# Kernel tuning notes

Measured on AMD Instinct MI355X. Metric: run time of the kernel, lower is better.

The kernel has to match this reference:

```python
import jax, jax.numpy as jnp
import numpy as np

D_MODEL = 1024
N_HEADS = 16
D_HEAD = D_MODEL // N_HEADS
D_FF = 4096
B, S = 4, 1024
EPS = 1e-12


def layer_norm(x, gamma, beta):
    # Faithful to the torch module: unbiased std (ddof=1) and division by (std + eps).
    mean = jnp.mean(x, axis=-1, keepdims=True)
    var = jnp.sum((x - mean) ** 2, axis=-1, keepdims=True) / (x.shape[-1] - 1)
    std = jnp.sqrt(var)
    return gamma * (x - mean) / (std + EPS) + beta


def setup_inputs() -> dict:
    key = jax.random.key(0)
    ks = jax.random.split(key, 10)
    sc = lambda fan_in: 1.0 / np.sqrt(fan_in)
    inp = {
        "x": jax.random.normal(ks[0], (B, S, D_MODEL), dtype=jnp.float32),
        "ln1_g": jnp.ones((D_MODEL,), jnp.float32),
        "ln1_b": jnp.zeros((D_MODEL,), jnp.float32),
        "wq": jax.random.normal(ks[1], (D_MODEL, D_MODEL), jnp.float32) * sc(D_MODEL),
        "bq": jnp.zeros((D_MODEL,), jnp.float32),
        "wk": jax.random.normal(ks[2], (D_MODEL, D_MODEL), jnp.float32) * sc(D_MODEL),
        "bk": jnp.zeros((D_MODEL,), jnp.float32),
        "wv": jax.random.normal(ks[3], (D_MODEL, D_MODEL), jnp.float32) * sc(D_MODEL),
        "bv": jnp.zeros((D_MODEL,), jnp.float32),
        "ln2_g": jnp.ones((D_MODEL,), jnp.float32),
        "ln2_b": jnp.zeros((D_MODEL,), jnp.float32),
        "w1": jax.random.normal(ks[4], (D_FF, D_MODEL), jnp.float32) * sc(D_MODEL),
        "b1": jnp.zeros((D_FF,), jnp.float32),
        "w2": jax.random.normal(ks[5], (D_MODEL, D_FF), jnp.float32) * sc(D_FF),
        "b2": jnp.zeros((D_MODEL,), jnp.float32),
    }
    return inp


def reference(x, ln1_g, ln1_b, wq, bq, wk, bk, wv, bv, ln2_g, ln2_b, w1, b1, w2, b2):
    Bsz, Sq, D = x.shape
    residual = x
    h = layer_norm(x, ln1_g, ln1_b)
    # QKV projections (no output projection in the original module)
    q = (h @ wq.T + bq).reshape(Bsz, Sq, N_HEADS, D_HEAD)
    k = (h @ wk.T + bk).reshape(Bsz, Sq, N_HEADS, D_HEAD)
    v = (h @ wv.T + bv).reshape(Bsz, Sq, N_HEADS, D_HEAD)
    scores = jnp.einsum("bqhd,bkhd->bhqk", q, k) / np.sqrt(D_HEAD)
    attn = jax.nn.softmax(scores, axis=-1)  # [B, H, S, S]
    ctx = jnp.einsum("bhqk,bkhd->bqhd", attn, v).reshape(Bsz, Sq, D)
    out = ctx + residual
    residual = out
    h2 = layer_norm(out, ln2_g, ln2_b)
    # 1x1 conv FFN == per-token MLP with ReLU (dropout inactive at eval)
    ff = jax.nn.relu(h2 @ w1.T + b1) @ w2.T + b2
    out = ff + residual
    # torch returns attn flattened head-major: [H*B, S, S]
    attn_ret = jnp.transpose(attn, (1, 0, 2, 3)).reshape(N_HEADS * Bsz, Sq, Sq)
    return out, attn_ret
```

## Files before the change

### kernel.cpp

```cpp
#include <hip/hip_runtime.h>
#include <cstdint>
#include <cstddef>

#define SEQ 1024
#define DM 1024
#define DF 4096
#define NH 16
#define DH 64
#define BSZ 4
#define NTOK (BSZ*SEQ)

typedef short s16x8 __attribute__((ext_vector_type(8)));
typedef float f32x4 __attribute__((ext_vector_type(4)));

__device__ __forceinline__ unsigned short f2bf(float f) {
  union { float f; unsigned u; } c; c.f = f;
  unsigned u = c.u;
  return (unsigned short)((u + 0x7fffu + ((u >> 16) & 1u)) >> 16);
}

__device__ __forceinline__ void gll16(const void* g, void* l) {
  __builtin_amdgcn_global_load_lds(
      (__attribute__((address_space(1))) void*)(g),
      (__attribute__((address_space(3))) void*)(l), 16, 0, 0);
}

template<int BM, int BN, int WM, int WN, int EPI>
__launch_bounds__(256)
__global__ void gemm_k(const unsigned short* __restrict__ A,
                       const unsigned short* __restrict__ W,
                       const float* __restrict__ bias,
                       void* __restrict__ outp,
                       const float* __restrict__ resid,
                       int nB, int K, int aRow, int wRow, int oRow,
                       long aY, long aZ, long wY, long wZ,
                       long oY, long oZ, long rY, long rZ, float scale) {
  constexpr int BK = 32;
  __shared__ unsigned short At[BM*BK];
  __shared__ unsigned short Wt[BN*BK];
  const int tid = threadIdx.x;
  const int mb = (int)blockIdx.x / nB, nb = (int)blockIdx.x % nB;
  const long aBase = (long)blockIdx.y*aY + (long)blockIdx.z*aZ + (long)mb*BM*aRow;
  const long wBase = (long)blockIdx.y*wY + (long)blockIdx.z*wZ + (long)nb*BN*wRow;
  const int wave = tid >> 6, lane = tid & 63;
  const int quad = lane >> 4, l16 = lane & 15;
  constexpr int WGN = BN / WN;
  const int wm = (wave / WGN) * WM, wn = (wave % WGN) * WN;
  constexpr int MT = WM/16, NT = WN/16;
  f32x4 acc[MT][NT] = {};
  const int srow = tid >> 2, skof = (tid & 3) * 8;

  for (int k0 = 0; k0 < K; k0 += BK) {
#pragma unroll
    for (int r = 0; r < BM; r += 64)
      gll16(A + aBase + (long)(r + srow)*aRow + k0 + skof, &At[(r + srow)*BK + skof]);
#pragma unroll
    for (int r = 0; r < BN; r += 64)
      gll16(W + wBase + (long)(r + srow)*wRow + k0 + skof, &Wt[(r + srow)*BK + skof]);
    __syncthreads();
    s16x8 af[MT];
#pragma unroll
    for (int mt = 0; mt < MT; ++mt)
      af[mt] = *(const s16x8*)&At[(wm + mt*16 + l16)*BK + quad*8];
#pragma unroll
    for (int nt = 0; nt < NT; ++nt) {
      s16x8 bfr = *(const s16x8*)&Wt[(wn + nt*16 + l16)*BK + quad*8];
#pragma unroll
      for (int mt = 0; mt < MT; ++mt)
        acc[mt][nt] = __builtin_amdgcn_mfma_f32_16x16x32_bf16(af[mt], bfr, acc[mt][nt], 0, 0, 0);
    }
    __syncthreads();
  }

  const long oBase = (long)blockIdx.y*oY + (long)blockIdx.z*oZ;
  const long rBase = (long)blockIdx.y*rY + (long)blockIdx.z*rZ;
#pragma unroll
  for (int mt = 0; mt < MT; ++mt) {
#pragma unroll
    for (int nt = 0; nt < NT; ++nt) {
      const int gn = nb*BN + wn + nt*16 + l16;
      const float bv = bias ? bias[gn] : 0.f;
#pragma unroll
      for (int r = 0; r < 4; ++r) {
        const int gm = mb*BM + wm + mt*16 + quad*4 + r;
        float v = acc[mt][nt][r] + bv;
        if (EPI == 0) {
          ((unsigned short*)outp)[oBase + (long)gm*oRow + gn] = f2bf(v * scale);
        } else if (EPI == 1) {
          ((unsigned short*)outp)[oBase + (long)gm*oRow + gn] = f2bf(v > 0.f ? v : 0.f);
        } else if (EPI == 2) {
          const int bb = gm >> 10, s = gm & 1023;
          ((unsigned short*)outp)[(long)bb*DM*SEQ + (long)gn*SEQ + s] = f2bf(v);
        } else if (EPI == 3) {
          const long o = oBase + (long)gm*oRow + gn;
          ((float*)outp)[o] = v + resid[rBase + (long)gm*oRow + gn];
        } else {
          ((float*)outp)[oBase + (long)gm*oRow + gn] = v;
        }
      }
    }
  }
}

__launch_bounds__(256)
__global__ void ln_k(const float* __restrict__ x, const float* __restrict__ g,
                     const float* __restrict__ bta, unsigned short* __restrict__ out) {
  const int row = blockIdx.x, t = threadIdx.x;
  const float4 v = ((const float4*)(x + (long)row*DM))[t];
  __shared__ float red[4];
  float s = v.x + v.y + v.z + v.w;
#pragma unroll
  for (int o = 32; o; o >>= 1) s += __shfl_down(s, o);
  if ((t & 63) == 0) red[t >> 6] = s;
  __syncthreads();
  const float mean = (red[0] + red[1] + red[2] + red[3]) * (1.f/1024.f);
  __syncthreads();
  const float dx = v.x - mean, dy = v.y - mean, dz = v.z - mean, dw = v.w - mean;
  float sq = dx*dx + dy*dy + dz*dz + dw*dw;
#pragma unroll
  for (int o = 32; o; o >>= 1) sq += __shfl_down(sq, o);
  if ((t & 63) == 0) red[t >> 6] = sq;
  __syncthreads();
  const float var = (red[0] + red[1] + red[2] + red[3]) * (1.f/1023.f);
  const float inv = 1.f / (sqrtf(var) + 1e-12f);
  const float4 gv = ((const float4*)g)[t];
  const float4 bv = ((const float4*)bta)[t];
  ushort4 o4;
  o4.x = f2bf(gv.x * dx * inv + bv.x);
  o4.y = f2bf(gv.y * dy * inv + bv.y);
  o4.z = f2bf(gv.z * dz * inv + bv.z);
  o4.w = f2bf(gv.w * dw * inv + bv.w);
  ((ushort4*)(out + (long)row*DM))[t] = o4;
}

__launch_bounds__(256)
__global__ void cvt_k(const float* __restrict__ in, unsigned short* __restrict__ out, int n4) {
  const int i = blockIdx.x*256 + threadIdx.x;
  if (i < n4) {
    const float4 v = ((const float4*)in)[i];
    ushort4 o; o.x = f2bf(v.x); o.y = f2bf(v.y); o.z = f2bf(v.z); o.w = f2bf(v.w);
    ((ushort4*)out)[i] = o;
  }
}

__launch_bounds__(256)
__global__ void attn_k(const unsigned short* __restrict__ Q,
                       const unsigned short* __restrict__ Kb,
                       float* __restrict__ attn_f,
                       unsigned short* __restrict__ attn_b) {
  const int b = blockIdx.y, h = blockIdx.z;
  const int q0 = blockIdx.x * 16;
  const int wave = threadIdx.x >> 6, lane = threadIdx.x & 63;
  const int quad = lane >> 4, l16 = lane & 15;
  const unsigned short* Qb = Q + (long)b*SEQ*DM + h*DH;
  const unsigned short* Kh = Kb + (long)b*SEQ*DM + h*DH;
  s16x8 af[2];
#pragma unroll
  for (int ks = 0; ks < 2; ++ks)
    af[ks] = *(const s16x8*)&Qb[(long)(q0 + l16)*DM + ks*32 + quad*8];
  f32x4 acc[16];
#pragma unroll
  for (int nt = 0; nt < 16; ++nt) acc[nt] = (f32x4){0.f, 0.f, 0.f, 0.f};
  for (int nt = 0; nt < 16; ++nt) {
    const int kc = wave*256 + nt*16 + l16;
#pragma unroll
    for (int ks = 0; ks < 2; ++ks) {
      const s16x8 bfr = *(const s16x8*)&Kh[(long)kc*DM + ks*32 + quad*8];
      acc[nt] = __builtin_amdgcn_mfma_f32_16x16x32_bf16(af[ks], bfr, acc[nt], 0, 0, 0);
    }
  }
  __shared__ float red[4][16];
  float rmax[4];
#pragma unroll
  for (int r = 0; r < 4; ++r) {
    float m = -3e38f;
#pragma unroll
    for (int nt = 0; nt < 16; ++nt) m = fmaxf(m, acc[nt][r]);
#pragma unroll
    for (int o = 1; o < 16; o <<= 1) m = fmaxf(m, __shfl_xor(m, o));
    rmax[r] = m;
  }
  if (l16 == 0) {
#pragma unroll
    for (int r = 0; r < 4; ++r) red[wave][quad*4 + r] = rmax[r];
  }
  __syncthreads();
#pragma unroll
  for (int r = 0; r < 4; ++r)
    rmax[r] = fmaxf(fmaxf(red[0][quad*4+r], red[1][quad*4+r]),
                    fmaxf(red[2][quad*4+r], red[3][quad*4+r]));
  __syncthreads();
#pragma unroll
  for (int r = 0; r < 4; ++r) {
    float s = 0.f;
#pragma unroll
    for (int nt = 0; nt < 16; ++nt) {
      const float e = __expf(acc[nt][r] - rmax[r]);
      acc[nt][r] = e; s += e;
    }
#pragma unroll
    for (int o = 1; o < 16; o <<= 1) s += __shfl_xor(s, o);
    if (l16 == 0) red[wave][quad*4 + r] = s;
  }
  __syncthreads();
  const long obase = (long)(h*BSZ + b)*SEQ*SEQ;
#pragma unroll
  for (int r = 0; r < 4; ++r) {
    const float tot = red[0][quad*4+r] + red[1][quad*4+r] + red[2][quad*4+r] + red[3][quad*4+r];
    const float inv = 1.f / tot;
    const long rowoff = obase + (long)(q0 + quad*4 + r)*SEQ;
#pragma unroll
    for (int nt = 0; nt < 16; ++nt) {
      const int col = wave*256 + nt*16 + l16;
      const float v = acc[nt][r] * inv;
      attn_f[rowoff + col] = v;
      attn_b[rowoff + col] = f2bf(v);
    }
  }
}

extern "C" void kernel_launch(void* const* d_in, const int* in_sizes, int n_in,
                              void* d_out, int out_size, void* d_ws, size_t ws_size,
                              hipStream_t stream) {
  const float* x    = (const float*)d_in[0];
  const float* ln1g = (const float*)d_in[1];
  const float* ln1b = (const float*)d_in[2];
  const float* wq   = (const float*)d_in[3];
  const float* bq   = (const float*)d_in[4];
  const float* wk   = (const float*)d_in[5];
  const float* bk   = (const float*)d_in[6];
  const float* wv   = (const float*)d_in[7];
  const float* bv   = (const float*)d_in[8];
  const float* ln2g = (const float*)d_in[9];
  const float* ln2b = (const float*)d_in[10];
  const float* w1   = (const float*)d_in[11];
  const float* b1   = (const float*)d_in[12];
  const float* w2   = (const float*)d_in[13];
  const float* b2   = (const float*)d_in[14];
  float* out    = (float*)d_out;
  float* attn_f = out + (long)NTOK*DM;

  uint8_t* p = (uint8_t*)d_ws;
  auto alloc = [&](size_t bytes) {
    uint8_t* r = p; p += (bytes + 255) & ~(size_t)255; return r;
  };
  unsigned short* hbuf  = (unsigned short*)alloc((size_t)NTOK*DM*2);
  unsigned short* qbuf  = (unsigned short*)alloc((size_t)NTOK*DM*2);
  unsigned short* kbuf  = (unsigned short*)alloc((size_t)NTOK*DM*2);
  unsigned short* vt    = (unsigned short*)alloc((size_t)BSZ*DM*SEQ*2);
  unsigned short* h2    = (unsigned short*)alloc((size_t)NTOK*DM*2);
  unsigned short* f1    = (unsigned short*)alloc((size_t)NTOK*DF*2);
  float*          out1  = (float*)alloc((size_t)NTOK*DM*4);
  unsigned short* attnb = (unsigned short*)alloc((size_t)NH*BSZ*SEQ*SEQ*2);
  unsigned short* wqb   = (unsigned short*)alloc((size_t)DM*DM*2);
  unsigned short* wkb   = (unsigned short*)alloc((size_t)DM*DM*2);
  unsigned short* wvb   = (unsigned short*)alloc((size_t)DM*DM*2);
  unsigned short* w1b   = (unsigned short*)alloc((size_t)DF*DM*2);
  unsigned short* w2b   = (unsigned short*)alloc((size_t)DM*DF*2);

  cvt_k<<<DM*DM/4/256, 256, 0, stream>>>(wq, wqb, DM*DM/4);
  cvt_k<<<DM*DM/4/256, 256, 0, stream>>>(wk, wkb, DM*DM/4);
  cvt_k<<<DM*DM/4/256, 256, 0, stream>>>(wv, wvb, DM*DM/4);
  cvt_k<<<DF*DM/4/256, 256, 0, stream>>>(w1, w1b, DF*DM/4);
  cvt_k<<<DM*DF/4/256, 256, 0, stream>>>(w2, w2b, DM*DF/4);

  ln_k<<<NTOK, 256, 0, stream>>>(x, ln1g, ln1b, hbuf);

  gemm_k<128,128,64,64,0><<<dim3((NTOK/128)*(DM/128)), 256, 0, stream>>>(
      hbuf, wqb, bq, qbuf, nullptr, DM/128, DM, DM, DM, DM,
      0,0,0,0,0,0,0,0, 0.125f);
  gemm_k<128,128,64,64,0><<<dim3((NTOK/128)*(DM/128)), 256, 0, stream>>>(
      hbuf, wkb, bk, kbuf, nullptr, DM/128, DM, DM, DM, DM,
      0,0,0,0,0,0,0,0, 1.f);
  gemm_k<128,128,64,64,2><<<dim3((NTOK/128)*(DM/128)), 256, 0, stream>>>(
      hbuf, wvb, bv, vt, nullptr, DM/128, DM, DM, DM, DM,
      0,0,0,0,0,0,0,0, 1.f);

  attn_k<<<dim3(SEQ/16, BSZ, NH), 256, 0, stream>>>(qbuf, kbuf, attn_f, attnb);

  gemm_k<128,64,32,64,3><<<dim3(SEQ/128, BSZ, NH), 256, 0, stream>>>(
      attnb, vt, nullptr, out1, x, 1, SEQ, SEQ, SEQ, DM,
      (long)SEQ*SEQ, (long)BSZ*SEQ*SEQ,
      (long)DM*SEQ, (long)DH*SEQ,
      (long)SEQ*DM, (long)DH,
      (long)SEQ*DM, (long)DH, 1.f);

  ln_k<<<NTOK, 256, 0, stream>>>(out1, ln2g, ln2b, h2);

  gemm_k<128,128,64,64,1><<<dim3((NTOK/128)*(DF/128)), 256, 0, stream>>>(
      h2, w1b, b1, f1, nullptr, DF/128, DM, DM, DM, DF,
      0,0,0,0,0,0,0,0, 1.f);

  gemm_k<128,128,64,64,3><<<dim3((NTOK/128)*(DM/128)), 256, 0, stream>>>(
      f1, w2b, b2, out, out1, DM/128, DF, DF, DF, DM,
      0,0,0,0,0,0,0,0, 1.f);
}
```

Before: 747.8 us.

## Fuse QKV GEMMs, weight conversions, and attention-times-V into attention kernel

After: 687.2 us. -8.1%, faster.

```diff
diff --git a/kernel.cpp b/kernel.cpp
--- a/kernel.cpp
+++ b/kernel.cpp
@@ -9,6 +9,7 @@
 #define DH 64
 #define BSZ 4
 #define NTOK (BSZ*SEQ)
+#define QKVSZ ((long)NTOK*DM)
 
 typedef short s16x8 __attribute__((ext_vector_type(8)));
 typedef float f32x4 __attribute__((ext_vector_type(4)));
@@ -17,6 +18,9 @@
   union { float f; unsigned u; } c; c.f = f;
   unsigned u = c.u;
   return (unsigned short)((u + 0x7fffu + ((u >> 16) & 1u)) >> 16);
+}
+__device__ __forceinline__ float bf2f(unsigned short b) {
+  union { unsigned u; float f; } c; c.u = ((unsigned)b) << 16; return c.f;
 }
 
 __device__ __forceinline__ void gll16(const void* g, void* l) {
@@ -33,15 +37,14 @@
                        void* __restrict__ outp,
                        const float* __restrict__ resid,
                        int nB, int K, int aRow, int wRow, int oRow,
-                       long aY, long aZ, long wY, long wZ,
-                       long oY, long oZ, long rY, long rZ, float scale) {
+                       float scale) {
   constexpr int BK = 32;
   __shared__ unsigned short At[BM*BK];
   __shared__ unsigned short Wt[BN*BK];
   const int tid = threadIdx.x;
   const int mb = (int)blockIdx.x / nB, nb = (int)blockIdx.x % nB;
-  const long aBase = (long)blockIdx.y*aY + (long)blockIdx.z*aZ + (long)mb*BM*aRow;
-  const long wBase = (long)blockIdx.y*wY + (long)blockIdx.z*wZ + (long)nb*BN*wRow;
+  const long aBase = (long)mb*BM*aRow;
+  const long wBase = (long)nb*BN*wRow;
   const int wave = tid >> 6, lane = tid & 63;
   const int quad = lane >> 4, l16 = lane & 15;
   constexpr int WGN = BN / WN;
@@ -72,8 +75,6 @@
     __syncthreads();
   }
 
-  const long oBase = (long)blockIdx.y*oY + (long)blockIdx.z*oZ;
-  const long rBase = (long)blockIdx.y*rY + (long)blockIdx.z*rZ;
 #pragma unroll
   for (int mt = 0; mt < MT; ++mt) {
 #pragma unroll
@@ -84,18 +85,22 @@
       for (int r = 0; r < 4; ++r) {
         const int gm = mb*BM + wm + mt*16 + quad*4 + r;
         float v = acc[mt][nt][r] + bv;
-        if (EPI == 0) {
-          ((unsigned short*)outp)[oBase + (long)gm*oRow + gn] = f2bf(v * scale);
-        } else if (EPI == 1) {
-          ((unsigned short*)outp)[oBase + (long)gm*oRow + gn] = f2bf(v > 0.f ? v : 0.f);
-        } else if (EPI == 2) {
-          const int bb = gm >> 10, s = gm & 1023;
-          ((unsigned short*)outp)[(long)bb*DM*SEQ + (long)gn*SEQ + s] = f2bf(v);
+        if (EPI == 1) {
+          ((unsigned short*)outp)[(long)gm*oRow + gn] = f2bf(v > 0.f ? v : 0.f);
         } else if (EPI == 3) {
-          const long o = oBase + (long)gm*oRow + gn;
-          ((float*)outp)[o] = v + resid[rBase + (long)gm*oRow + gn];
-        } else {
-          ((float*)outp)[oBase + (long)gm*oRow + gn] = v;
+          const long o = (long)gm*oRow + gn;
+          ((float*)outp)[o] = v + resid[o];
+        } else if (EPI == 5) {
+          unsigned short* base = (unsigned short*)outp;
+          const int reg = gn >> 10, cn = gn & 1023;
+          if (reg == 0) {
+            base[(long)gm*DM + cn] = f2bf(v * scale);
+          } else if (reg == 1) {
+            base[QKVSZ + (long)gm*DM + cn] = f2bf(v);
+          } else {
+            const int bb = gm >> 10, s = gm & 1023;
+            base[2*QKVSZ + (long)bb*DM*SEQ + (long)cn*SEQ + s] = f2bf(v);
+          }
         }
       }
     }
@@ -133,25 +138,55 @@
   ((ushort4*)(out + (long)row*DM))[t] = o4;
 }
 
+#define R_WQ  262144L
+#define R_WK  524288L
+#define R_WV  786432L
+#define R_W1  1835008L
+#define R_W2  2883584L
+#define CVT_BLOCKS 11265
 __launch_bounds__(256)
-__global__ void cvt_k(const float* __restrict__ in, unsigned short* __restrict__ out, int n4) {
-  const int i = blockIdx.x*256 + threadIdx.x;
-  if (i < n4) {
-    const float4 v = ((const float4*)in)[i];
-    ushort4 o; o.x = f2bf(v.x); o.y = f2bf(v.y); o.z = f2bf(v.z); o.w = f2bf(v.w);
-    ((ushort4*)out)[i] = o;
-  }
-}
-
+__global__ void cvt5_k(const float* __restrict__ wq, const float* __restrict__ wk,
+                       const float* __restrict__ wv, const float* __restrict__ w1,
+                       const float* __restrict__ w2,
+                       const float* __restrict__ bq, const float* __restrict__ bk,
+                       const float* __restrict__ bvv,
+                       unsigned short* __restrict__ wqkvb,
+                       unsigned short* __restrict__ w1b,
+                       unsigned short* __restrict__ w2b,
+                       float* __restrict__ bcat) {
+  const long blk = blockIdx.x;
+  if (blk == CVT_BLOCKS - 1) {
+    for (int j = threadIdx.x; j < 3072; j += 256)
+      bcat[j] = j < 1024 ? bq[j] : (j < 2048 ? bk[j - 1024] : bvv[j - 2048]);
+    return;
+  }
+  long i = blk*256 + threadIdx.x;
+  const float* s; unsigned short* d;
+  if (i < R_WQ)       { s = wq; d = wqkvb;              }
+  else if (i < R_WK)  { s = wk; d = wqkvb + 1048576; i -= R_WQ; }
+  else if (i < R_WV)  { s = wv; d = wqkvb + 2097152; i -= R_WK; }
+  else if (i < R_W1)  { s = w1; d = w1b;             i -= R_WV; }
+  else                { s = w2; d = w2b;             i -= R_W1; }
+  const float4 v = ((const float4*)s)[i];
+  ushort4 o; o.x = f2bf(v.x); o.y = f2bf(v.y); o.z = f2bf(v.z); o.w = f2bf(v.w);
+  ((ushort4*)d)[i] = o;
+}
+
+#define LDP 1032
 __launch_bounds__(256)
 __global__ void attn_k(const unsigned short* __restrict__ Q,
                        const unsigned short* __restrict__ Kb,
+                       const unsigned short* __restrict__ vt,
+                       const float* __restrict__ xres,
                        float* __restrict__ attn_f,
-                       unsigned short* __restrict__ attn_b) {
+                       float* __restrict__ out1) {
   const int b = blockIdx.y, h = blockIdx.z;
   const int q0 = blockIdx.x * 16;
   const int wave = threadIdx.x >> 6, lane = threadIdx.x & 63;
   const int quad = lane >> 4, l16 = lane & 15;
+  __shared__ unsigned short PL[16 * LDP];
+  __shared__ float red[4][16];
+
   const unsigned short* Qb = Q + (long)b*SEQ*DM + h*DH;
   const unsigned short* Kh = Kb + (long)b*SEQ*DM + h*DH;
   s16x8 af[2];
@@ -169,7 +204,7 @@
       acc[nt] = __builtin_amdgcn_mfma_f32_16x16x32_bf16(af[ks], bfr, acc[nt], 0, 0, 0);
     }
   }
-  __shared__ float red[4][16];
+
   float rmax[4];
 #pragma unroll
   for (int r = 0; r < 4; ++r) {
@@ -203,19 +238,45 @@
     if (l16 == 0) red[wave][quad*4 + r] = s;
   }
   __syncthreads();
-  const long obase = (long)(h*BSZ + b)*SEQ*SEQ;
+
 #pragma unroll
   for (int r = 0; r < 4; ++r) {
     const float tot = red[0][quad*4+r] + red[1][quad*4+r] + red[2][quad*4+r] + red[3][quad*4+r];
     const float inv = 1.f / tot;
-    const long rowoff = obase + (long)(q0 + quad*4 + r)*SEQ;
-#pragma unroll
-    for (int nt = 0; nt < 16; ++nt) {
-      const int col = wave*256 + nt*16 + l16;
-      const float v = acc[nt][r] * inv;
-      attn_f[rowoff + col] = v;
-      attn_b[rowoff + col] = f2bf(v);
-    }
+    unsigned short* prow = &PL[(quad*4 + r)*LDP + wave*256 + l16];
+#pragma unroll
+    for (int nt = 0; nt < 16; ++nt)
+      prow[nt*16] = f2bf(acc[nt][r] * inv);
+  }
+  __syncthreads();
+
+  {
+    const long obase = (long)(h*BSZ + b)*SEQ*SEQ + (long)q0*SEQ;
+    const int col = threadIdx.x * 4;
+#pragma unroll
+    for (int row = 0; row < 16; ++row) {
+      const ushort4 pv = *(const ushort4*)&PL[row*LDP + col];
+      float4 o;
+      o.x = bf2f(pv.x); o.y = bf2f(pv.y); o.z = bf2f(pv.z); o.w = bf2f(pv.w);
+      ((float4*)(attn_f + obase + (long)row*SEQ))[threadIdx.x] = o;
+    }
+  }
+
+  f32x4 c = (f32x4){0.f, 0.f, 0.f, 0.f};
+  const unsigned short* Vh = vt + (long)b*DM*SEQ + (long)(h*DH + wave*16 + l16)*SEQ;
+#pragma unroll 4
+  for (int k0 = 0; k0 < 32; ++k0) {
+    const s16x8 a  = *(const s16x8*)&PL[l16*LDP + k0*32 + quad*8];
+    const s16x8 bf = *(const s16x8*)&Vh[k0*32 + quad*8];
+    c = __builtin_amdgcn_mfma_f32_16x16x32_bf16(a, bf, c, 0, 0, 0);
+  }
+
+#pragma unroll
+  for (int r = 0; r < 4; ++r) {
+    const int gq = q0 + quad*4 + r;
+    const int col = h*DH + wave*16 + l16;
+    const long idx = (long)b*SEQ*DM + (long)gq*DM + col;
+    out1[idx] = c[r] + xres[idx];
   }
 }
 
@@ -245,53 +306,30 @@
     uint8_t* r = p; p += (bytes + 255) & ~(size_t)255; return r;
   };
   unsigned short* hbuf  = (unsigned short*)alloc((size_t)NTOK*DM*2);
-  unsigned short* qbuf  = (unsigned short*)alloc((size_t)NTOK*DM*2);
-  unsigned short* kbuf  = (unsigned short*)alloc((size_t)NTOK*DM*2);
-  unsigned short* vt    = (unsigned short*)alloc((size_t)BSZ*DM*SEQ*2);
+  unsigned short* qkv   = (unsigned short*)alloc((size_t)3*NTOK*DM*2);
   unsigned short* h2    = (unsigned short*)alloc((size_t)NTOK*DM*2);
   unsigned short* f1    = (unsigned short*)alloc((size_t)NTOK*DF*2);
   float*          out1  = (float*)alloc((size_t)NTOK*DM*4);
-  unsigned short* attnb = (unsigned short*)alloc((size_t)NH*BSZ*SEQ*SEQ*2);
-  unsigned short* wqb   = (unsigned short*)alloc((size_t)DM*DM*2);
-  unsigned short* wkb   = (unsigned short*)alloc((size_t)DM*DM*2);
-  unsigned short* wvb   = (unsigned short*)alloc((size_t)DM*DM*2);
+  unsigned short* wqkvb = (unsigned short*)alloc((size_t)3*DM*DM*2);
   unsigned short* w1b   = (unsigned short*)alloc((size_t)DF*DM*2);
   unsigned short* w2b   = (unsigned short*)alloc((size_t)DM*DF*2);
-
-  cvt_k<<<DM*DM/4/256, 256, 0, stream>>>(wq, wqb, DM*DM/4);
-  cvt_k<<<DM*DM/4/256, 256, 0, stream>>>(wk, wkb, DM*DM/4);
-  cvt_k<<<DM*DM/4/256, 256, 0, stream>>>(wv, wvb, DM*DM/4);
-  cvt_k<<<DF*DM/4/256, 256, 0, stream>>>(w1, w1b, DF*DM/4);
-  cvt_k<<<DM*DF/4/256, 256, 0, stream>>>(w2, w2b, DM*DF/4);
-
+  float*          bcat  = (float*)alloc((size_t)3*DM*4);
+
+  cvt5_k<<<CVT_BLOCKS, 256, 0, stream>>>(wq, wk, wv, w1, w2, bq, bk, bv,
+                                         wqkvb, w1b, w2b, bcat);
   ln_k<<<NTOK, 256, 0, stream>>>(x, ln1g, ln1b, hbuf);
 
-  gemm_k<128,128,64,64,0><<<dim3((NTOK/128)*(DM/128)), 256, 0, stream>>>(
-      hbuf, wqb, bq, qbuf, nullptr, DM/128, DM, DM, DM, DM,
-      0,0,0,0,0,0,0,0, 0.125f);
-  gemm_k<128,128,64,64,0><<<dim3((NTOK/128)*(DM/128)), 256, 0, stream>>>(
-      hbuf, wkb, bk, kbuf, nullptr, DM/128, DM, DM, DM, DM,
-      0,0,0,0,0,0,0,0, 1.f);
-  gemm_k<128,128,64,64,2><<<dim3((NTOK/128)*(DM/128)), 256, 0, stream>>>(
-      hbuf, wvb, bv, vt, nullptr, DM/128, DM, DM, DM, DM,
-      0,0,0,0,0,0,0,0, 1.f);
-
-  attn_k<<<dim3(SEQ/16, BSZ, NH), 256, 0, stream>>>(qbuf, kbuf, attn_f, attnb);
-
-  gemm_k<128,64,32,64,3><<<dim3(SEQ/128, BSZ, NH), 256, 0, stream>>>(
-      attnb, vt, nullptr, out1, x, 1, SEQ, SEQ, SEQ, DM,
-      (long)SEQ*SEQ, (long)BSZ*SEQ*SEQ,
-      (long)DM*SEQ, (long)DH*SEQ,
-      (long)SEQ*DM, (long)DH,
-      (long)SEQ*DM, (long)DH, 1.f);
+  gemm_k<128,128,64,64,5><<<dim3((NTOK/128)*(3*DM/128)), 256, 0, stream>>>(
+      hbuf, wqkvb, bcat, qkv, nullptr, 3*DM/128, DM, DM, DM, DM, 0.125f);
+
+  attn_k<<<dim3(SEQ/16, BSZ, NH), 256, 0, stream>>>(
+      qkv, qkv + QKVSZ, qkv + 2*QKVSZ, x, attn_f, out1);
 
   ln_k<<<NTOK, 256, 0, stream>>>(out1, ln2g, ln2b, h2);
 
   gemm_k<128,128,64,64,1><<<dim3((NTOK/128)*(DF/128)), 256, 0, stream>>>(
-      h2, w1b, b1, f1, nullptr, DF/128, DM, DM, DM, DF,
-      0,0,0,0,0,0,0,0, 1.f);
+      h2, w1b, b1, f1, nullptr, DF/128, DM, DM, DM, DF, 1.f);
 
   gemm_k<128,128,64,64,3><<<dim3((NTOK/128)*(DM/128)), 256, 0, stream>>>(
-      f1, w2b, b2, out, out1, DM/128, DF, DF, DF, DM,
-      0,0,0,0,0,0,0,0, 1.f);
-}
+      f1, w2b, b2, out, out1, DM/128, DF, DF, DF, DM, 1.f);
+}
```
